# Kernel tuning notes

Hardware: AMD Instinct MI355X
Metric: run time of the kernel (lower is better)

Reference implementation:

```python
import jax, jax.numpy as jnp
import numpy as np

B, T, NUM_SKILLS, CONCEPT_NUM, HIDDEN = 64, 200, 1024, 256, 1024


def setup_inputs() -> dict:
    key = jax.random.key(0)
    ks = jax.random.split(key, 12)
    s_in = 1.0 / np.sqrt(NUM_SKILLS)
    s_h = 1.0 / np.sqrt(HIDDEN)
    s_c = 1.0 / np.sqrt(CONCEPT_NUM)
    return {
        "q_hot": jax.random.normal(ks[0], (B, T, NUM_SKILLS), jnp.float32),
        "result": jax.random.randint(ks[1], (B, T), 0, 2, jnp.int32),
        "next_q_hot": jax.random.normal(ks[2], (B, T, NUM_SKILLS), jnp.float32),
        "concept_num": CONCEPT_NUM,
        # kc: Linear(num_skills -> concept_num)
        "W_kc": jax.random.uniform(ks[3], (CONCEPT_NUM, NUM_SKILLS), jnp.float32, -s_in, s_in),
        "b_kc": jax.random.uniform(ks[4], (CONCEPT_NUM,), jnp.float32, -s_in, s_in),
        # LSTM (input = 2*concept_num, hidden = HIDDEN), torch gate order i,f,g,o
        "W_ih": jax.random.uniform(ks[5], (4 * HIDDEN, 2 * CONCEPT_NUM), jnp.float32, -s_h, s_h),
        "W_hh": jax.random.uniform(ks[6], (4 * HIDDEN, HIDDEN), jnp.float32, -s_h, s_h),
        "b_ih": jax.random.uniform(ks[7], (4 * HIDDEN,), jnp.float32, -s_h, s_h),
        "b_hh": jax.random.uniform(ks[8], (4 * HIDDEN,), jnp.float32, -s_h, s_h),
        # state: Linear(hidden -> concept_num)
        "W_state": jax.random.uniform(ks[9], (CONCEPT_NUM, HIDDEN), jnp.float32, -s_h, s_h),
        "b_state": jax.random.uniform(ks[10], (CONCEPT_NUM,), jnp.float32, -s_h, s_h),
        # out: Linear(concept_num -> 1)
        "W_out": jax.random.uniform(ks[11], (1, CONCEPT_NUM), jnp.float32, -s_c, s_c),
        "b_out": jax.random.uniform(jax.random.fold_in(key, 99), (1,), jnp.float32, -s_c, s_c),
    }


def _lstm(x, W_ih, W_hh, b_ih, b_hh):
    # x: [B, T, In] batch_first; returns h_seq [B, T, H]
    H = W_hh.shape[1]
    xT = jnp.swapaxes(x, 0, 1)                      # [T, B, In]
    gx = jnp.einsum('tbi,gi->tbg', xT, W_ih) + b_ih + b_hh  # [T, B, 4H]
    h0 = jnp.zeros((x.shape[0], H), x.dtype)
    c0 = jnp.zeros((x.shape[0], H), x.dtype)

    def step(carry, g_t):
        h, c = carry
        g = g_t + h @ W_hh.T                        # [B, 4H]
        i, f, gg, o = jnp.split(g, 4, axis=-1)
        i, f, o = jax.nn.sigmoid(i), jax.nn.sigmoid(f), jax.nn.sigmoid(o)
        c = f * c + i * jnp.tanh(gg)
        h = o * jnp.tanh(c)
        return (h, c), h

    _, h_seq = jax.lax.scan(step, (h0, c0), gx)
    return jnp.swapaxes(h_seq, 0, 1)                # [B, T, H]


def reference(q_hot, result, next_q_hot, concept_num,
              W_kc, b_kc, W_ih, W_hh, b_ih, b_hh,
              W_state, b_state, W_out, b_out):
    kc_hot = q_hot @ W_kc.T + b_kc                  # [B, T, C]
    next_kc_hot = next_q_hot @ W_kc.T + b_kc        # [B, T, C]

    # Vectorized replacement of the python double loop:
    # result==1 -> [kc_hot, 0]; else -> [0, kc_hot]
    mask = (result == 1)[..., None].astype(kc_hot.dtype)  # [B, T, 1]
    kc_vec = jnp.concatenate([kc_hot * mask, kc_hot * (1.0 - mask)], axis=-1)  # [B,T,2C]

    h = _lstm(kc_vec, W_ih, W_hh, b_ih, b_hh)       # [B, T, H]
    stu_state = h @ W_state.T + b_state             # [B, T, C]
    knowledge_div = stu_state - next_kc_hot
    vector = knowledge_div * next_kc_hot
    res = vector @ W_out.T + b_out                  # [B, T, 1]
    return (res, stu_state)
```

## Files before the change

kernel.cpp:

```cpp
#include <hip/hip_runtime.h>
#include <math.h>


typedef unsigned short u16;
typedef unsigned long long u64;
typedef __bf16 bf16x8 __attribute__((ext_vector_type(8)));
typedef float floatx4 __attribute__((ext_vector_type(4)));
typedef unsigned int u32x4 __attribute__((ext_vector_type(4)));

__device__ __forceinline__ float bf2f(u16 h) {
  unsigned int u = ((unsigned int)h) << 16;
  float f;
  __builtin_memcpy(&f, &u, 4);
  return f;
}
__device__ __forceinline__ u16 f2bf(float f) {
  unsigned int u;
  __builtin_memcpy(&u, &f, 4);
  u += 0x7FFFu + ((u >> 16) & 1u);
  return (u16)(u >> 16);
}
__device__ __forceinline__ float sigm(float x) { return 1.0f / (1.0f + __expf(-x)); }

__global__ void cvt_kernel(const float* __restrict__ in, u16* __restrict__ out) {
  const int i = blockIdx.x * 256 + threadIdx.x;
  const float4 v = ((const float4*)in)[i];
  ushort4 o;
  o.x = f2bf(v.x);
  o.y = f2bf(v.y);
  o.z = f2bf(v.z);
  o.w = f2bf(v.w);
  ((ushort4*)out)[i] = o;
}

template <class Epi>
__global__ __launch_bounds__(256, 2) void gemm_bt(const u16* __restrict__ A,
                                                  const u16* __restrict__ B,
                                                  int M, int N, int K, Epi epi) {
  __shared__ u16 As[128 * 32];
  __shared__ u16 Bs[128 * 32];
  const int tid = threadIdx.x;
  const int w = tid >> 6, lane = tid & 63;
  const int wm = w & 1, wn = w >> 1;
  const int bm = blockIdx.x * 128, bn = blockIdx.y * 128;
  const int lrow = lane & 15, lk8 = (lane >> 4) * 8;
  const int srow = lane >> 2;
  const int skc = (lane & 3) * 8;

  floatx4 acc[4][4] = {};

  for (int k0 = 0; k0 < K; k0 += 32) {
#pragma unroll
    for (int r = 0; r < 2; ++r) {
      const int seg = w * 2 + r;
      const int row = seg * 16 + srow;
      __builtin_amdgcn_global_load_lds(
          (const __attribute__((address_space(1))) unsigned int*)(A + (size_t)(bm + row) * K + k0 + skc),
          (__attribute__((address_space(3))) unsigned int*)(As + seg * 512), 16, 0, 0);
      __builtin_amdgcn_global_load_lds(
          (const __attribute__((address_space(1))) unsigned int*)(B + (size_t)(bn + row) * K + k0 + skc),
          (__attribute__((address_space(3))) unsigned int*)(Bs + seg * 512), 16, 0, 0);
    }
    __syncthreads();

    bf16x8 af[4], bfr[4];
#pragma unroll
    for (int i = 0; i < 4; ++i) {
      af[i] = *(const bf16x8*)(As + (wm * 64 + i * 16 + lrow) * 32 + lk8);
      bfr[i] = *(const bf16x8*)(Bs + (wn * 64 + i * 16 + lrow) * 32 + lk8);
    }
#pragma unroll
    for (int i = 0; i < 4; ++i)
#pragma unroll
      for (int j = 0; j < 4; ++j)
        acc[i][j] = __builtin_amdgcn_mfma_f32_16x16x32_bf16(af[i], bfr[j], acc[i][j], 0, 0, 0);
    __syncthreads();
  }

  const int rbase = bm + wm * 64 + (lane >> 4) * 4;
  const int cbase = bn + wn * 64 + lrow;
#pragma unroll
  for (int i = 0; i < 4; ++i)
#pragma unroll
    for (int j = 0; j < 4; ++j)
#pragma unroll
      for (int r = 0; r < 4; ++r)
        epi(rbase + i * 16 + r, cbase + j * 16, acc[i][j][r]);
}

struct EpiKcVec {
  const float* bkc;
  const int* result;
  u16* kcv;
  __device__ void operator()(int row, int col, float v) const {
    v += bkc[col];
    const int off = (result[row] == 1) ? 0 : 256;
    const size_t base = (size_t)row * 512;
    kcv[base + off + col] = f2bf(v);
    kcv[base + (256 - off) + col] = 0;
  }
};
struct EpiNk {
  const float* bkc;
  float* nk;
  __device__ void operator()(int row, int col, float v) const {
    nk[(size_t)row * 256 + col] = v + bkc[col];
  }
};
struct EpiGx {
  const float* bih;
  const float* bhh;
  u16* gx;
  __device__ void operator()(int row, int col, float v) const {
    v += bih[col] + bhh[col];
    const int b = row / 200, t = row - b * 200;
    gx[(size_t)(t * 64 + b) * 4096 + col] = f2bf(v);
  }
};
struct EpiStu {
  const float* bst;
  float* out;
  __device__ void operator()(int row, int col, float v) const {
    v += bst[col];
    const int b = row & 63, t = row >> 6;
    out[(size_t)(b * 200 + t) * 256 + col] = v;
  }
};

__global__ void init_kernel(u16* hseq, unsigned* flags) {
  const int i = blockIdx.x * 256 + threadIdx.x;
  ((u64*)hseq)[i] = 0ULL;
  if (blockIdx.x == 0 && threadIdx.x < 128) flags[threadIdx.x] = 0u;
}

__global__ __launch_bounds__(512, 2) void lstm_scan(const u16* __restrict__ Whh,
                                                    const u16* __restrict__ gx,
                                                    u16* __restrict__ hseq,
                                                    unsigned* __restrict__ flags) {
  __shared__ __align__(16) u16 Ab[16 * 1032];
  __shared__ float gbuf[4 * 512];
  __shared__ __align__(16) u16 hbuf[16 * 32];
  const int tid = threadIdx.x;
  const int w = tid >> 6;
  const int lane = tid & 63;
  const int lrow = lane & 15;
  const int lk8 = (lane >> 4) * 8;
  const int g = w & 3;
  const int hf = w >> 2;
  const int gb = blockIdx.x >> 5;
  const int gn = blockIdx.x & 31;
  const int bb = gb * 16;
  const int j0 = gn * 32;

  bf16x8 bfrag[32];
  {
    const u16* wp = Whh + (size_t)(g * 1024 + j0 + hf * 16 + lrow) * 1024 + lk8;
#pragma unroll
    for (int ks = 0; ks < 32; ++ks) bfrag[ks] = *(const bf16x8*)(wp + ks * 32);
  }

  float c_state = 0.0f;
  const int um = tid >> 5, un = tid & 31;

  const u16* gxb =
      gx + (size_t)(bb + (lane >> 4) * 4) * 4096 + g * 1024 + j0 + hf * 16 + lrow;
  u16 gcur[4];
  {
    const u16* gp = gxb;
    gcur[0] = gp[0];
    gcur[1] = gp[4096];
    gcur[2] = gp[8192];
    gcur[3] = gp[12288];
  }

  for (int t = 0; t < 200; ++t) {
    {
      const char* hb = (const char*)(hseq + (size_t)t * 65536 + (size_t)bb * 1024);
      const char* p0 = hb + tid * 16;
      const char* p1 = p0 + 8192;
      const char* p2 = p0 + 16384;
      const char* p3 = p0 + 24576;
      u32x4 t0, t1, t2, t3;
      asm volatile(
          "global_load_dwordx4 %0, %4, off sc0 sc1\n\t"
          "global_load_dwordx4 %1, %5, off sc0 sc1\n\t"
          "global_load_dwordx4 %2, %6, off sc0 sc1\n\t"
          "global_load_dwordx4 %3, %7, off sc0 sc1\n\t"
          "s_waitcnt vmcnt(0)"
          : "=&v"(t0), "=&v"(t1), "=&v"(t2), "=&v"(t3)
          : "v"(p0), "v"(p1), "v"(p2), "v"(p3)
          : "memory");
      {
        const int ch = tid;
        *(u32x4*)(Ab + (ch >> 7) * 1032 + (ch & 127) * 8) = t0;
      }
      {
        const int ch = 512 + tid;
        *(u32x4*)(Ab + (ch >> 7) * 1032 + (ch & 127) * 8) = t1;
      }
      {
        const int ch = 1024 + tid;
        *(u32x4*)(Ab + (ch >> 7) * 1032 + (ch & 127) * 8) = t2;
      }
      {
        const int ch = 1536 + tid;
        *(u32x4*)(Ab + (ch >> 7) * 1032 + (ch & 127) * 8) = t3;
      }
    }
    __syncthreads();

    floatx4 a0, a1 = {}, a2 = {}, a3 = {};
    a0[0] = bf2f(gcur[0]);
    a0[1] = bf2f(gcur[1]);
    a0[2] = bf2f(gcur[2]);
    a0[3] = bf2f(gcur[3]);

    if (t < 199) {
      const u16* gp = gxb + (size_t)(t + 1) * 262144;
      gcur[0] = gp[0];
      gcur[1] = gp[4096];
      gcur[2] = gp[8192];
      gcur[3] = gp[12288];
    }

#pragma unroll
    for (int ks = 0; ks < 32; ks += 4) {
      const u16* ap = Ab + lrow * 1032 + ks * 32 + lk8;
      a0 = __builtin_amdgcn_mfma_f32_16x16x32_bf16(*(const bf16x8*)(ap), bfrag[ks], a0, 0, 0, 0);
      a1 = __builtin_amdgcn_mfma_f32_16x16x32_bf16(*(const bf16x8*)(ap + 32), bfrag[ks + 1], a1, 0, 0, 0);
      a2 = __builtin_amdgcn_mfma_f32_16x16x32_bf16(*(const bf16x8*)(ap + 64), bfrag[ks + 2], a2, 0, 0, 0);
      a3 = __builtin_amdgcn_mfma_f32_16x16x32_bf16(*(const bf16x8*)(ap + 96), bfrag[ks + 3], a3, 0, 0, 0);
    }
    const floatx4 acc = (a0 + a1) + (a2 + a3);
    {
      const int mrow = (lane >> 4) * 4;
#pragma unroll
      for (int r = 0; r < 4; ++r)
        gbuf[g * 512 + (mrow + r) * 32 + hf * 16 + lrow] = acc[r];
    }
    __syncthreads();

    const float gi = gbuf[um * 32 + un];
    const float gf = gbuf[512 + um * 32 + un];
    const float gg = gbuf[1024 + um * 32 + un];
    const float go = gbuf[1536 + um * 32 + un];
    c_state = sigm(gf) * c_state + sigm(gi) * tanhf(gg);
    const float h = sigm(go) * tanhf(c_state);
    hbuf[um * 32 + un] = f2bf(h);
    __syncthreads();

    if (tid < 64) {
#pragma unroll
      for (int k = 0; k < 2; ++k) {
        const int wi = k * 64 + lane;
        const int row = wi >> 3, cw = wi & 7;
        const u64 v = *(const u64*)(hbuf + row * 32 + cw * 4);
        u64 old = __hip_atomic_exchange(
            (u64*)(hseq + (size_t)(t + 1) * 65536 + (size_t)(bb + row) * 1024 +
                   j0 + cw * 4),
            v, __ATOMIC_RELAXED, __HIP_MEMORY_SCOPE_AGENT);
        asm volatile("" ::"v"(old));
      }
      asm volatile("s_waitcnt vmcnt(0)" ::: "memory");
      if (lane == 0)
        __hip_atomic_store(&flags[blockIdx.x], (unsigned)(t + 1), __ATOMIC_RELAXED,
                           __HIP_MEMORY_SCOPE_AGENT);

      const unsigned tgt = (unsigned)(t + 1);
      const unsigned* gfp = &flags[gb * 32 + (lane & 31)];
      for (;;) {
        const unsigned v = __hip_atomic_load(gfp, __ATOMIC_RELAXED,
                                             __HIP_MEMORY_SCOPE_AGENT);
        if (__all(v >= tgt)) break;
        __builtin_amdgcn_s_sleep(1);
      }
    }
    __syncthreads();
  }
}

__global__ void res_kernel(const float* __restrict__ stu, const float* __restrict__ nk,
                           const float* __restrict__ Wout, const float* __restrict__ bout,
                           float* __restrict__ res) {
  const int row = blockIdx.x * 4 + (threadIdx.x >> 6);
  const int lane = threadIdx.x & 63;
  const float* sp = stu + (size_t)row * 256;
  const float* np = nk + (size_t)row * 256;
  float s = 0.0f;
#pragma unroll
  for (int j = 0; j < 4; ++j) {
    const int c = j * 64 + lane;
    const float nv = np[c];
    s += (sp[c] - nv) * nv * Wout[c];
  }
#pragma unroll
  for (int o = 32; o > 0; o >>= 1) s += __shfl_down(s, o, 64);
  if (lane == 0) res[row] = s + bout[0];
}

extern "C" void kernel_launch(void* const* d_in, const int* in_sizes, int n_in,
                              void* d_out, int out_size, void* d_ws, size_t ws_size,
                              hipStream_t stream) {
  const float* q_hot = (const float*)d_in[0];
  const int* result = (const int*)d_in[1];
  const float* next_q = (const float*)d_in[2];
  const float* W_kc = (const float*)d_in[4];
  const float* b_kc = (const float*)d_in[5];
  const float* W_ih = (const float*)d_in[6];
  const float* W_hh = (const float*)d_in[7];
  const float* b_ih = (const float*)d_in[8];
  const float* b_hh = (const float*)d_in[9];
  const float* W_state = (const float*)d_in[10];
  const float* b_state = (const float*)d_in[11];
  const float* W_out = (const float*)d_in[12];
  const float* b_out = (const float*)d_in[13];

  float* out_res = (float*)d_out;
  float* out_stu = out_res + 12800;

  char* ws = (char*)d_ws;
  u16* kcv = (u16*)(ws);
  float* nk = (float*)(ws + 13107200);
  u16* hseq = (u16*)(ws + 26214400);
  u16* Whh_bf = (u16*)(ws + 52559872);
  u16* Wih_bf = (u16*)(ws + 60948480);
  u16* Wkc_bf = (u16*)(ws + 65142784);
  u16* Wst_bf = (u16*)(ws + 65667072);
  unsigned* flags = (unsigned*)(ws + 66191360);
  u16* gx = (u16*)(ws + 66192384);
  u16* q_bf = gx;
  u16* nq_bf = gx + 13107200;

  cvt_kernel<<<dim3(12800), 256, 0, stream>>>(q_hot, q_bf);
  cvt_kernel<<<dim3(12800), 256, 0, stream>>>(next_q, nq_bf);
  cvt_kernel<<<dim3(256), 256, 0, stream>>>(W_kc, Wkc_bf);
  cvt_kernel<<<dim3(2048), 256, 0, stream>>>(W_ih, Wih_bf);
  cvt_kernel<<<dim3(4096), 256, 0, stream>>>(W_hh, Whh_bf);
  cvt_kernel<<<dim3(256), 256, 0, stream>>>(W_state, Wst_bf);

  init_kernel<<<dim3(64), 256, 0, stream>>>(hseq, flags);
  gemm_bt<EpiKcVec><<<dim3(100, 2), 256, 0, stream>>>(q_bf, Wkc_bf, 12800, 256, 1024,
                                                      EpiKcVec{b_kc, result, kcv});
  gemm_bt<EpiNk><<<dim3(100, 2), 256, 0, stream>>>(nq_bf, Wkc_bf, 12800, 256, 1024,
                                                   EpiNk{b_kc, nk});
  gemm_bt<EpiGx><<<dim3(100, 32), 256, 0, stream>>>(kcv, Wih_bf, 12800, 4096, 512,
                                                    EpiGx{b_ih, b_hh, gx});
  lstm_scan<<<dim3(128), 512, 0, stream>>>(Whh_bf, gx, hseq, flags);
  gemm_bt<EpiStu><<<dim3(100, 2), 256, 0, stream>>>(hseq + 65536, Wst_bf, 12800, 256, 1024,
                                                    EpiStu{b_state, out_stu});
  res_kernel<<<dim3(3200), 256, 0, stream>>>(out_stu, nk, W_out, b_out, out_res);
}
```

Before: 1.268 ms.

## Restructure LSTM scan to 64 larger blocks with counter-based group barrier

Each scan block now owns 64 hidden units with 1024 threads instead of 32 units with 512 threads, halving the number of blocks per batch group. The per-block flag array and single-wave polling barrier are replaced by one atomic counter per batch group, incremented by every wave after its h write and spun on by all threads at the next step. The hbuf staging and an extra __syncthreads are removed, since waves write h directly via shuffles. This reduces synchronization overhead per step, at the cost of less CU parallelism and more contention on a single counter.

```diff
diff --git a/kernel.cpp b/kernel.cpp
--- a/kernel.cpp
+++ b/kernel.cpp
@@ -127,43 +127,42 @@
   }
 };
 
-__global__ void init_kernel(u16* hseq, unsigned* flags) {
+__global__ void init_kernel(u16* hseq, unsigned* cnt) {
   const int i = blockIdx.x * 256 + threadIdx.x;
   ((u64*)hseq)[i] = 0ULL;
-  if (blockIdx.x == 0 && threadIdx.x < 128) flags[threadIdx.x] = 0u;
-}
-
-__global__ __launch_bounds__(512, 2) void lstm_scan(const u16* __restrict__ Whh,
-                                                    const u16* __restrict__ gx,
-                                                    u16* __restrict__ hseq,
-                                                    unsigned* __restrict__ flags) {
+  if (blockIdx.x == 0 && threadIdx.x < 128) cnt[threadIdx.x] = 0u;
+}
+
+__global__ __launch_bounds__(1024, 1) void lstm_scan(const u16* __restrict__ Whh,
+                                                     const u16* __restrict__ gx,
+                                                     u16* __restrict__ hseq,
+                                                     unsigned* __restrict__ cnt) {
   __shared__ __align__(16) u16 Ab[16 * 1032];
-  __shared__ float gbuf[4 * 512];
-  __shared__ __align__(16) u16 hbuf[16 * 32];
+  __shared__ float gbuf[4 * 16 * 64];
   const int tid = threadIdx.x;
   const int w = tid >> 6;
   const int lane = tid & 63;
   const int lrow = lane & 15;
   const int lk8 = (lane >> 4) * 8;
   const int g = w & 3;
-  const int hf = w >> 2;
-  const int gb = blockIdx.x >> 5;
-  const int gn = blockIdx.x & 31;
+  const int cq = w >> 2;
+  const int gb = blockIdx.x >> 4;
+  const int gn = blockIdx.x & 15;
   const int bb = gb * 16;
-  const int j0 = gn * 32;
+  const int j0 = gn * 64;
+  unsigned* const gcnt = cnt + gb * 16;
 
   bf16x8 bfrag[32];
   {
-    const u16* wp = Whh + (size_t)(g * 1024 + j0 + hf * 16 + lrow) * 1024 + lk8;
+    const u16* wp = Whh + (size_t)(g * 1024 + j0 + cq * 16 + lrow) * 1024 + lk8;
 #pragma unroll
     for (int ks = 0; ks < 32; ++ks) bfrag[ks] = *(const bf16x8*)(wp + ks * 32);
   }
 
   float c_state = 0.0f;
-  const int um = tid >> 5, un = tid & 31;
 
   const u16* gxb =
-      gx + (size_t)(bb + (lane >> 4) * 4) * 4096 + g * 1024 + j0 + hf * 16 + lrow;
+      gx + (size_t)(bb + (lane >> 4) * 4) * 4096 + g * 1024 + j0 + cq * 16 + lrow;
   u16 gcur[4];
   {
     const u16* gp = gxb;
@@ -174,37 +173,35 @@
   }
 
   for (int t = 0; t < 200; ++t) {
+    if (t > 0) {
+      const unsigned tgt = (unsigned)t * 256u;
+      for (unsigned spin = 0; spin < (1u << 20); ++spin) {
+        const unsigned v = __hip_atomic_load(gcnt, __ATOMIC_RELAXED,
+                                             __HIP_MEMORY_SCOPE_AGENT);
+        if (v >= tgt) break;
+        __builtin_amdgcn_s_sleep(1);
+      }
+    }
+
     {
       const char* hb = (const char*)(hseq + (size_t)t * 65536 + (size_t)bb * 1024);
       const char* p0 = hb + tid * 16;
-      const char* p1 = p0 + 8192;
-      const char* p2 = p0 + 16384;
-      const char* p3 = p0 + 24576;
-      u32x4 t0, t1, t2, t3;
+      const char* p1 = p0 + 16384;
+      u32x4 t0, t1;
       asm volatile(
-          "global_load_dwordx4 %0, %4, off sc0 sc1\n\t"
-          "global_load_dwordx4 %1, %5, off sc0 sc1\n\t"
-          "global_load_dwordx4 %2, %6, off sc0 sc1\n\t"
-          "global_load_dwordx4 %3, %7, off sc0 sc1\n\t"
+          "global_load_dwordx4 %0, %2, off sc0 sc1\n\t"
+          "global_load_dwordx4 %1, %3, off sc0 sc1\n\t"
           "s_waitcnt vmcnt(0)"
-          : "=&v"(t0), "=&v"(t1), "=&v"(t2), "=&v"(t3)
-          : "v"(p0), "v"(p1), "v"(p2), "v"(p3)
+          : "=&v"(t0), "=&v"(t1)
+          : "v"(p0), "v"(p1)
           : "memory");
       {
         const int ch = tid;
         *(u32x4*)(Ab + (ch >> 7) * 1032 + (ch & 127) * 8) = t0;
       }
       {
-        const int ch = 512 + tid;
+        const int ch = 1024 + tid;
         *(u32x4*)(Ab + (ch >> 7) * 1032 + (ch & 127) * 8) = t1;
-      }
-      {
-        const int ch = 1024 + tid;
-        *(u32x4*)(Ab + (ch >> 7) * 1032 + (ch & 127) * 8) = t2;
-      }
-      {
-        const int ch = 1536 + tid;
-        *(u32x4*)(Ab + (ch >> 7) * 1032 + (ch & 127) * 8) = t3;
       }
     }
     __syncthreads();
@@ -236,46 +233,37 @@
       const int mrow = (lane >> 4) * 4;
 #pragma unroll
       for (int r = 0; r < 4; ++r)
-        gbuf[g * 512 + (mrow + r) * 32 + hf * 16 + lrow] = acc[r];
+        gbuf[g * 1024 + (mrow + r) * 64 + cq * 16 + lrow] = acc[r];
     }
     __syncthreads();
 
-    const float gi = gbuf[um * 32 + un];
-    const float gf = gbuf[512 + um * 32 + un];
-    const float gg = gbuf[1024 + um * 32 + un];
-    const float go = gbuf[1536 + um * 32 + un];
+    const float gi = gbuf[w * 64 + lane];
+    const float gf = gbuf[1024 + w * 64 + lane];
+    const float gg = gbuf[2048 + w * 64 + lane];
+    const float go = gbuf[3072 + w * 64 + lane];
     c_state = sigm(gf) * c_state + sigm(gi) * tanhf(gg);
     const float h = sigm(go) * tanhf(c_state);
-    hbuf[um * 32 + un] = f2bf(h);
-    __syncthreads();
-
-    if (tid < 64) {
-#pragma unroll
-      for (int k = 0; k < 2; ++k) {
-        const int wi = k * 64 + lane;
-        const int row = wi >> 3, cw = wi & 7;
-        const u64 v = *(const u64*)(hbuf + row * 32 + cw * 4);
-        u64 old = __hip_atomic_exchange(
-            (u64*)(hseq + (size_t)(t + 1) * 65536 + (size_t)(bb + row) * 1024 +
-                   j0 + cw * 4),
-            v, __ATOMIC_RELAXED, __HIP_MEMORY_SCOPE_AGENT);
+
+    {
+      const unsigned hb16 = (unsigned)f2bf(h);
+      const unsigned nb = (unsigned)__shfl_xor((int)hb16, 1, 64);
+      const unsigned lo = (lane & 1) ? (nb | (hb16 << 16)) : (hb16 | (nb << 16));
+      const unsigned hi = (unsigned)__shfl_xor((int)lo, 2, 64);
+      if ((lane & 3) == 0) {
+        const u64 word = (u64)lo | ((u64)hi << 32);
+        u64* dst = (u64*)(hseq + (size_t)(t + 1) * 65536 + (size_t)(bb + w) * 1024 + j0) +
+                   (lane >> 2);
+        u64 old = __hip_atomic_exchange(dst, word, __ATOMIC_RELAXED,
+                                        __HIP_MEMORY_SCOPE_AGENT);
         asm volatile("" ::"v"(old));
       }
       asm volatile("s_waitcnt vmcnt(0)" ::: "memory");
-      if (lane == 0)
-        __hip_atomic_store(&flags[blockIdx.x], (unsigned)(t + 1), __ATOMIC_RELAXED,
-                           __HIP_MEMORY_SCOPE_AGENT);
-
-      const unsigned tgt = (unsigned)(t + 1);
-      const unsigned* gfp = &flags[gb * 32 + (lane & 31)];
-      for (;;) {
-        const unsigned v = __hip_atomic_load(gfp, __ATOMIC_RELAXED,
-                                             __HIP_MEMORY_SCOPE_AGENT);
-        if (__all(v >= tgt)) break;
-        __builtin_amdgcn_s_sleep(1);
-      }
-    }
-    __syncthreads();
+      if (lane == 0) {
+        unsigned o = __hip_atomic_fetch_add(gcnt, 1u, __ATOMIC_RELAXED,
+                                            __HIP_MEMORY_SCOPE_AGENT);
+        asm volatile("" ::"v"(o));
+      }
+    }
   }
 }
 
@@ -326,7 +314,7 @@
   u16* Wih_bf = (u16*)(ws + 60948480);
   u16* Wkc_bf = (u16*)(ws + 65142784);
   u16* Wst_bf = (u16*)(ws + 65667072);
-  unsigned* flags = (unsigned*)(ws + 66191360);
+  unsigned* cnt = (unsigned*)(ws + 66191360);
   u16* gx = (u16*)(ws + 66192384);
   u16* q_bf = gx;
   u16* nq_bf = gx + 13107200;
@@ -338,14 +326,14 @@
   cvt_kernel<<<dim3(4096), 256, 0, stream>>>(W_hh, Whh_bf);
   cvt_kernel<<<dim3(256), 256, 0, stream>>>(W_state, Wst_bf);
 
-  init_kernel<<<dim3(64), 256, 0, stream>>>(hseq, flags);
+  init_kernel<<<dim3(64), 256, 0, stream>>>(hseq, cnt);
   gemm_bt<EpiKcVec><<<dim3(100, 2), 256, 0, stream>>>(q_bf, Wkc_bf, 12800, 256, 1024,
                                                       EpiKcVec{b_kc, result, kcv});
   gemm_bt<EpiNk><<<dim3(100, 2), 256, 0, stream>>>(nq_bf, Wkc_bf, 12800, 256, 1024,
                                                    EpiNk{b_kc, nk});
   gemm_bt<EpiGx><<<dim3(100, 32), 256, 0, stream>>>(kcv, Wih_bf, 12800, 4096, 512,
                                                     EpiGx{b_ih, b_hh, gx});
-  lstm_scan<<<dim3(128), 512, 0, stream>>>(Whh_bf, gx, hseq, flags);
+  lstm_scan<<<dim3(64), 1024, 0, stream>>>(Whh_bf, gx, hseq, cnt);
   gemm_bt<EpiStu><<<dim3(100, 2), 256, 0, stream>>>(hseq + 65536, Wst_bf, 12800, 256, 1024,
                                                     EpiStu{b_state, out_stu});
   res_kernel<<<dim3(3200), 256, 0, stream>>>(out_stu, nk, W_out, b_out, out_res);
```

Result: slower. 4.165 ms (+228.6%).

## Interleave two batch chains per LSTM block to hide inter-block sync latency

Applied to the files above, without the earlier changes.

Each LSTM scan block now handles two 16-row batch chains and alternates between them, cutting the grid from 128 to 64 blocks. While one chain waits on the flags of its 32-block column group, the other chain's step can run, so the cross-block barrier latency overlaps with useful work. The spin wait is now bounded by an iteration limit. The cost is fewer CUs in use and twice as much serial work per block, and the iteration cap could end the wait early and read stale h values.

```diff
diff --git a/kernel.cpp b/kernel.cpp
--- a/kernel.cpp
+++ b/kernel.cpp
@@ -147,10 +147,13 @@
   const int lk8 = (lane >> 4) * 8;
   const int g = w & 3;
   const int hf = w >> 2;
-  const int gb = blockIdx.x >> 5;
-  const int gn = blockIdx.x & 31;
-  const int bb = gb * 16;
-  const int j0 = gn * 32;
+  const int sg = blockIdx.x >> 5;
+  const int cg = blockIdx.x & 31;
+  const int j0 = cg * 32;
+  const int bbA = sg * 32;
+  const int bbB = sg * 32 + 16;
+  const int fA = (sg * 2 + 0) * 32;
+  const int fB = (sg * 2 + 1) * 32;
 
   bf16x8 bfrag[32];
   {
@@ -159,123 +162,141 @@
     for (int ks = 0; ks < 32; ++ks) bfrag[ks] = *(const bf16x8*)(wp + ks * 32);
   }
 
-  float c_state = 0.0f;
+  float cA = 0.0f, cB = 0.0f;
   const int um = tid >> 5, un = tid & 31;
 
-  const u16* gxb =
-      gx + (size_t)(bb + (lane >> 4) * 4) * 4096 + g * 1024 + j0 + hf * 16 + lrow;
-  u16 gcur[4];
+  const u16* gxbA =
+      gx + (size_t)(bbA + (lane >> 4) * 4) * 4096 + g * 1024 + j0 + hf * 16 + lrow;
+  const u16* gxbB = gxbA + (size_t)16 * 4096;
+  u16 gcA[4], gcB[4];
   {
-    const u16* gp = gxb;
-    gcur[0] = gp[0];
-    gcur[1] = gp[4096];
-    gcur[2] = gp[8192];
-    gcur[3] = gp[12288];
+    gcA[0] = gxbA[0];
+    gcA[1] = gxbA[4096];
+    gcA[2] = gxbA[8192];
+    gcA[3] = gxbA[12288];
+    gcB[0] = gxbB[0];
+    gcB[1] = gxbB[4096];
+    gcB[2] = gxbB[8192];
+    gcB[3] = gxbB[12288];
   }
 
   for (int t = 0; t < 200; ++t) {
-    {
-      const char* hb = (const char*)(hseq + (size_t)t * 65536 + (size_t)bb * 1024);
-      const char* p0 = hb + tid * 16;
-      const char* p1 = p0 + 8192;
-      const char* p2 = p0 + 16384;
-      const char* p3 = p0 + 24576;
-      u32x4 t0, t1, t2, t3;
-      asm volatile(
-          "global_load_dwordx4 %0, %4, off sc0 sc1\n\t"
-          "global_load_dwordx4 %1, %5, off sc0 sc1\n\t"
-          "global_load_dwordx4 %2, %6, off sc0 sc1\n\t"
-          "global_load_dwordx4 %3, %7, off sc0 sc1\n\t"
-          "s_waitcnt vmcnt(0)"
-          : "=&v"(t0), "=&v"(t1), "=&v"(t2), "=&v"(t3)
-          : "v"(p0), "v"(p1), "v"(p2), "v"(p3)
-          : "memory");
+#pragma unroll
+    for (int chain = 0; chain < 2; ++chain) {
+      const int bb = chain ? bbB : bbA;
+      u16* gc = chain ? gcB : gcA;
+      const u16* gxb = chain ? gxbB : gxbA;
+
       {
-        const int ch = tid;
-        *(u32x4*)(Ab + (ch >> 7) * 1032 + (ch & 127) * 8) = t0;
-      }
+        const char* hb = (const char*)(hseq + (size_t)t * 65536 + (size_t)bb * 1024);
+        const char* p0 = hb + tid * 16;
+        const char* p1 = p0 + 8192;
+        const char* p2 = p0 + 16384;
+        const char* p3 = p0 + 24576;
+        u32x4 t0, t1, t2, t3;
+        asm volatile(
+            "global_load_dwordx4 %0, %4, off sc0 sc1\n\t"
+            "global_load_dwordx4 %1, %5, off sc0 sc1\n\t"
+            "global_load_dwordx4 %2, %6, off sc0 sc1\n\t"
+            "global_load_dwordx4 %3, %7, off sc0 sc1\n\t"
+            "s_waitcnt vmcnt(0)"
+            : "=&v"(t0), "=&v"(t1), "=&v"(t2), "=&v"(t3)
+            : "v"(p0), "v"(p1), "v"(p2), "v"(p3)
+            : "memory");
+        {
+          const int ch = tid;
+          *(u32x4*)(Ab + (ch >> 7) * 1032 + (ch & 127) * 8) = t0;
+        }
+        {
+          const int ch = 512 + tid;
+          *(u32x4*)(Ab + (ch >> 7) * 1032 + (ch & 127) * 8) = t1;
+        }
+        {
+          const int ch = 1024 + tid;
+          *(u32x4*)(Ab + (ch >> 7) * 1032 + (ch & 127) * 8) = t2;
+        }
+        {
+          const int ch = 1536 + tid;
+          *(u32x4*)(Ab + (ch >> 7) * 1032 + (ch & 127) * 8) = t3;
+        }
+      }
+      __syncthreads();
+
+      floatx4 a0, a1 = {}, a2 = {}, a3 = {};
+      a0[0] = bf2f(gc[0]);
+      a0[1] = bf2f(gc[1]);
+      a0[2] = bf2f(gc[2]);
+      a0[3] = bf2f(gc[3]);
+
+      if (t < 199) {
+        const u16* gp = gxb + (size_t)(t + 1) * 262144;
+        gc[0] = gp[0];
+        gc[1] = gp[4096];
+        gc[2] = gp[8192];
+        gc[3] = gp[12288];
+      }
+
+#pragma unroll
+      for (int ks = 0; ks < 32; ks += 4) {
+        const u16* ap = Ab + lrow * 1032 + ks * 32 + lk8;
+        a0 = __builtin_amdgcn_mfma_f32_16x16x32_bf16(*(const bf16x8*)(ap), bfrag[ks], a0, 0, 0, 0);
+        a1 = __builtin_amdgcn_mfma_f32_16x16x32_bf16(*(const bf16x8*)(ap + 32), bfrag[ks + 1], a1, 0, 0, 0);
+        a2 = __builtin_amdgcn_mfma_f32_16x16x32_bf16(*(const bf16x8*)(ap + 64), bfrag[ks + 2], a2, 0, 0, 0);
+        a3 = __builtin_amdgcn_mfma_f32_16x16x32_bf16(*(const bf16x8*)(ap + 96), bfrag[ks + 3], a3, 0, 0, 0);
+      }
+      const floatx4 acc = (a0 + a1) + (a2 + a3);
       {
-        const int ch = 512 + tid;
-        *(u32x4*)(Ab + (ch >> 7) * 1032 + (ch & 127) * 8) = t1;
-      }
+        const int mrow = (lane >> 4) * 4;
+#pragma unroll
+        for (int r = 0; r < 4; ++r)
+          gbuf[g * 512 + (mrow + r) * 32 + hf * 16 + lrow] = acc[r];
+      }
+      __syncthreads();
+
       {
-        const int ch = 1024 + tid;
-        *(u32x4*)(Ab + (ch >> 7) * 1032 + (ch & 127) * 8) = t2;
-      }
-      {
-        const int ch = 1536 + tid;
-        *(u32x4*)(Ab + (ch >> 7) * 1032 + (ch & 127) * 8) = t3;
-      }
+        const float gi = gbuf[um * 32 + un];
+        const float gf = gbuf[512 + um * 32 + un];
+        const float gg = gbuf[1024 + um * 32 + un];
+        const float go = gbuf[1536 + um * 32 + un];
+        float c = chain ? cB : cA;
+        c = sigm(gf) * c + sigm(gi) * tanhf(gg);
+        const float h = sigm(go) * tanhf(c);
+        if (chain)
+          cB = c;
+        else
+          cA = c;
+        hbuf[um * 32 + un] = f2bf(h);
+      }
+      __syncthreads();
+
+      if (tid < 64) {
+#pragma unroll
+        for (int k = 0; k < 2; ++k) {
+          const int wi = k * 64 + lane;
+          const int row = wi >> 3, cw = wi & 7;
+          const u64 v = *(const u64*)(hbuf + row * 32 + cw * 4);
+          u64 old = __hip_atomic_exchange(
+              (u64*)(hseq + (size_t)(t + 1) * 65536 + (size_t)(bb + row) * 1024 +
+                     j0) + cw,
+              v, __ATOMIC_RELAXED, __HIP_MEMORY_SCOPE_AGENT);
+          asm volatile("" ::"v"(old));
+        }
+        asm volatile("s_waitcnt vmcnt(0)" ::: "memory");
+        if (lane == 0)
+          __hip_atomic_store(&flags[(chain ? fB : fA) + cg], (unsigned)(t + 1),
+                             __ATOMIC_RELAXED, __HIP_MEMORY_SCOPE_AGENT);
+
+        const unsigned tgt = chain ? (unsigned)(t + 1) : (unsigned)t;
+        const unsigned* gfp = &flags[(chain ? fA : fB) + (lane & 31)];
+        for (unsigned spin = 0; spin < (1u << 20); ++spin) {
+          const unsigned v = __hip_atomic_load(gfp, __ATOMIC_RELAXED,
+                                               __HIP_MEMORY_SCOPE_AGENT);
+          if (__all(v >= tgt)) break;
+          __builtin_amdgcn_s_sleep(1);
+        }
+      }
+      __syncthreads();
     }
-    __syncthreads();
-
-    floatx4 a0, a1 = {}, a2 = {}, a3 = {};
-    a0[0] = bf2f(gcur[0]);
-    a0[1] = bf2f(gcur[1]);
-    a0[2] = bf2f(gcur[2]);
-    a0[3] = bf2f(gcur[3]);
-
-    if (t < 199) {
-      const u16* gp = gxb + (size_t)(t + 1) * 262144;
-      gcur[0] = gp[0];
-      gcur[1] = gp[4096];
-      gcur[2] = gp[8192];
-      gcur[3] = gp[12288];
-    }
-
-#pragma unroll
-    for (int ks = 0; ks < 32; ks += 4) {
-      const u16* ap = Ab + lrow * 1032 + ks * 32 + lk8;
-      a0 = __builtin_amdgcn_mfma_f32_16x16x32_bf16(*(const bf16x8*)(ap), bfrag[ks], a0, 0, 0, 0);
-      a1 = __builtin_amdgcn_mfma_f32_16x16x32_bf16(*(const bf16x8*)(ap + 32), bfrag[ks + 1], a1, 0, 0, 0);
-      a2 = __builtin_amdgcn_mfma_f32_16x16x32_bf16(*(const bf16x8*)(ap + 64), bfrag[ks + 2], a2, 0, 0, 0);
-      a3 = __builtin_amdgcn_mfma_f32_16x16x32_bf16(*(const bf16x8*)(ap + 96), bfrag[ks + 3], a3, 0, 0, 0);
-    }
-    const floatx4 acc = (a0 + a1) + (a2 + a3);
-    {
-      const int mrow = (lane >> 4) * 4;
-#pragma unroll
-      for (int r = 0; r < 4; ++r)
-        gbuf[g * 512 + (mrow + r) * 32 + hf * 16 + lrow] = acc[r];
-    }
-    __syncthreads();
-
-    const float gi = gbuf[um * 32 + un];
-    const float gf = gbuf[512 + um * 32 + un];
-    const float gg = gbuf[1024 + um * 32 + un];
-    const float go = gbuf[1536 + um * 32 + un];
-    c_state = sigm(gf) * c_state + sigm(gi) * tanhf(gg);
-    const float h = sigm(go) * tanhf(c_state);
-    hbuf[um * 32 + un] = f2bf(h);
-    __syncthreads();
-
-    if (tid < 64) {
-#pragma unroll
-      for (int k = 0; k < 2; ++k) {
-        const int wi = k * 64 + lane;
-        const int row = wi >> 3, cw = wi & 7;
-        const u64 v = *(const u64*)(hbuf + row * 32 + cw * 4);
-        u64 old = __hip_atomic_exchange(
-            (u64*)(hseq + (size_t)(t + 1) * 65536 + (size_t)(bb + row) * 1024 +
-                   j0 + cw * 4),
-            v, __ATOMIC_RELAXED, __HIP_MEMORY_SCOPE_AGENT);
-        asm volatile("" ::"v"(old));
-      }
-      asm volatile("s_waitcnt vmcnt(0)" ::: "memory");
-      if (lane == 0)
-        __hip_atomic_store(&flags[blockIdx.x], (unsigned)(t + 1), __ATOMIC_RELAXED,
-                           __HIP_MEMORY_SCOPE_AGENT);
-
-      const unsigned tgt = (unsigned)(t + 1);
-      const unsigned* gfp = &flags[gb * 32 + (lane & 31)];
-      for (;;) {
-        const unsigned v = __hip_atomic_load(gfp, __ATOMIC_RELAXED,
-                                             __HIP_MEMORY_SCOPE_AGENT);
-        if (__all(v >= tgt)) break;
-        __builtin_amdgcn_s_sleep(1);
-      }
-    }
-    __syncthreads();
   }
 }
 
@@ -345,7 +366,7 @@
                                                    EpiNk{b_kc, nk});
   gemm_bt<EpiGx><<<dim3(100, 32), 256, 0, stream>>>(kcv, Wih_bf, 12800, 4096, 512,
                                                     EpiGx{b_ih, b_hh, gx});
-  lstm_scan<<<dim3(128), 512, 0, stream>>>(Whh_bf, gx, hseq, flags);
+  lstm_scan<<<dim3(64), 512, 0, stream>>>(Whh_bf, gx, hseq, flags);
   gemm_bt<EpiStu><<<dim3(100, 2), 256, 0, stream>>>(hseq + 65536, Wst_bf, 12800, 256, 1024,
                                                     EpiStu{b_state, out_stu});
   res_kernel<<<dim3(3200), 256, 0, stream>>>(out_stu, nk, W_out, b_out, out_res);
```

Result: slower. 1.717 ms (+35.4%).
